# Performance work log

Measured on AMD Instinct MI355X. Metric: run time of the kernel, lower is better.

Reference implementation:

```python
import jax, jax.numpy as jnp
from jax import lax
import numpy as np

GRID = 16
N = GRID * GRID  # 256 nodes
D = 64           # embed_dim
CLIP = 3.0
EPS = 1e-8

def _grid_structs():
    mask = np.zeros((N, N), dtype=np.float32)
    first_nb = np.zeros(N, dtype=np.int64)
    for i in range(N):
        r, c = divmod(i, GRID)
        nbs = []
        if r > 0: nbs.append(i - GRID)
        if r < GRID - 1: nbs.append(i + GRID)
        if c > 0: nbs.append(i - 1)
        if c < GRID - 1: nbs.append(i + 1)
        for n in nbs:
            mask[i, n] = 1.0
        first_nb[i] = nbs[0]
    fn_onehot = np.zeros((N, N), dtype=bool)
    fn_onehot[np.arange(N), first_nb] = True
    return mask, fn_onehot

_ADJ_MASK_NP, _FN_ONEHOT_NP = _grid_structs()
_FN_ONEHOT = jnp.asarray(_FN_ONEHOT_NP)

def setup_inputs() -> dict:
    key = jax.random.key(0)
    ks = jax.random.split(key, 12)
    B, F, H, C = 4096, 512, D * N, 1000
    s = lambda fan: 1.0 / np.sqrt(fan)
    return {
        'x': jax.random.normal(ks[0], (B, F), jnp.float32),
        'W_in': jax.random.normal(ks[1], (H, F), jnp.float32) * s(F),
        'b_in': jnp.zeros((H,), jnp.float32),
        'adj_weights': jax.random.normal(ks[2], (N, N), jnp.float32) * 0.1,
        'adj_mask': jnp.asarray(_ADJ_MASK_NP),
        'V_slow': jax.random.normal(ks[3], (D, D), jnp.float32) * 0.1,
        'sem_mem': jax.random.normal(ks[4], (D, D), jnp.float32) * 0.01,
        'mix_w': jax.random.normal(ks[5], (1, D), jnp.float32) * s(D),
        'mix_b': jnp.zeros((1,), jnp.float32),
        'basis': jax.random.normal(ks[6], (4, D), jnp.float32) * 0.5,
        'q_w': jax.random.normal(ks[7], (D, D), jnp.float32) * s(D),
        'q_b': jnp.zeros((D,), jnp.float32),
        'k_w': jax.random.normal(ks[8], (D, D), jnp.float32) * s(D),
        'k_b': jnp.zeros((D,), jnp.float32),
        'W_out': jax.random.normal(ks[9], (C, H), jnp.float32) * s(H),
        'b_out': jnp.zeros((C,), jnp.float32),
    }

def reference(x, W_in, b_in, adj_weights, adj_mask, V_slow, sem_mem,
              mix_w, mix_b, basis, q_w, q_b, k_w, k_b, W_out, b_out):
    B = x.shape[0]
    # input embedding -> [B, N, D] node states
    nodes = (x @ W_in.T + b_in).reshape(B, N, D)

    # --- StableTopologyManager.get_adjacency (plasticity = 1.0) ---
    adj = jax.nn.sigmoid(adj_weights) * adj_mask          # [N, N]
    deg = jnp.clip(adj.sum(1, keepdims=True), 1e-6, None)
    adj = adj / deg
    # min-connections survival protocol (vectorized)
    need = (adj > 0.1).sum(1) < 1                         # [N]
    adj = jnp.where(need[:, None] & _FN_ONEHOT, jnp.maximum(adj, 0.5), adj)

    # grid message passing: aggregate neighbor states
    nodes = jnp.einsum('nm,bmd->bnd', adj, nodes)

    # --- StableContinuumMemoryCell (output path; EMA state update is no_grad
    # and does not affect this forward's output) ---
    v = jnp.clip(nodes @ V_slow.T, -CLIP, CLIP)
    y_pred = jnp.clip(nodes @ sem_mem.T, -CLIP, CLIP)
    v_pred = jnp.clip(y_pred @ V_slow.T, -CLIP, CLIP)
    mix = jax.nn.sigmoid(lax.stop_gradient(v) @ mix_w.T + mix_b)  # [B,N,1]
    cell_out = jnp.clip(mix * v + (1.0 - mix) * v_pred, -CLIP, CLIP)

    # --- StableSymbioticBasisRefinement ---
    Q = cell_out @ q_w.T + q_b                            # [B,N,D]
    K = basis @ k_w.T + k_b                               # [4,D]
    attn = (Q @ K.T) / (D ** 0.5 + EPS)                   # [B,N,4]
    w = jax.nn.softmax(attn, axis=-1)
    x_clean = jnp.clip(w @ basis, -3.0, 3.0)              # [B,N,D]

    # readout
    flat = x_clean.reshape(B, N * D)
    logits = flat @ W_out.T + b_out                       # [B, 1000]
    return logits
```

## Files before the change

kernel.cpp:

```cpp
#include <hip/hip_runtime.h>
#include <stdint.h>
#include <stddef.h>


typedef __attribute__((ext_vector_type(8))) __bf16 bf16x8;
typedef __attribute__((ext_vector_type(4))) float  floatx4;

#define N_NODES 256
#define F_IN    512
#define B_BATCH 4096
#define C_OUT   1000
#define NT      9
#define SCOLS   (N_NODES * NT)
#define KPACK   (N_NODES * 4)
#define OUT_N   4096000

__device__ __forceinline__ unsigned short f2us(float f) {
  unsigned int v; __builtin_memcpy(&v, &f, sizeof(v));
  unsigned int r = (v + 0x7FFFu + ((v >> 16) & 1u)) >> 16;
  return (unsigned short)r;
}
__device__ __forceinline__ float us2f(unsigned short u) {
  unsigned int v = ((unsigned int)u) << 16;
  float f; __builtin_memcpy(&f, &v, sizeof(f)); return f;
}
__device__ __forceinline__ void async_ld16(const void* g, void* l) {
  __builtin_amdgcn_global_load_lds(
      (const __attribute__((address_space(1))) unsigned int*)g,
      (__attribute__((address_space(3))) unsigned int*)l, 16, 0, 0);
}

__global__ __launch_bounds__(256)
void setup_kernel(const float* __restrict__ adj_w,
                  const float* __restrict__ basis,
                  const float* __restrict__ q_w,
                  const float* __restrict__ q_b,
                  const float* __restrict__ k_w,
                  const float* __restrict__ k_b,
                  const float* __restrict__ V_slow,
                  const float* __restrict__ sem_mem,
                  const float* __restrict__ mix_w,
                  const float* __restrict__ mix_b,
                  const float* __restrict__ b_in,
                  const float* __restrict__ b_out,
                  float* __restrict__ adjw, int* __restrict__ adjidx,
                  float* __restrict__ vecs,
                  float* __restrict__ qbK,
                  float* __restrict__ misc,
                  float* __restrict__ bias9,
                  float* __restrict__ biasc)
{
  __shared__ float K4[4 * 64];
  __shared__ float KQ[4 * 64];
  __shared__ float A1s[4 * 64];
  __shared__ float vecsS[9 * 64];
  __shared__ float adjwS[256 * 4];
  __shared__ int   adjidxS[256 * 4];
  const int tid = threadIdx.x;

  for (int i = tid; i < C_OUT; i += 256) biasc[i] = b_out[i];

  {
    const int n = tid, r = n >> 4, c = n & 15;
    int nb[4]; int cnt = 0;
    if (r > 0)  nb[cnt++] = n - 16;
    if (r < 15) nb[cnt++] = n + 16;
    if (c > 0)  nb[cnt++] = n - 1;
    if (c < 15) nb[cnt++] = n + 1;
    float wv[4] = {0.f, 0.f, 0.f, 0.f};
    float s = 0.f;
    for (int i = 0; i < cnt; ++i) {
      float sg = 1.f / (1.f + expf(-adj_w[(size_t)n * 256 + nb[i]]));
      wv[i] = sg; s += sg;
    }
    float deg = fmaxf(s, 1e-6f);
    int over = 0;
    for (int i = 0; i < cnt; ++i) { wv[i] /= deg; over += (wv[i] > 0.1f) ? 1 : 0; }
    if (over < 1) wv[0] = fmaxf(wv[0], 0.5f);
    for (int i = cnt; i < 4; ++i) nb[i] = n;
    for (int i = 0; i < 4; ++i) {
      adjw[n * 4 + i] = wv[i];  adjidx[n * 4 + i] = nb[i];
      adjwS[n * 4 + i] = wv[i]; adjidxS[n * 4 + i] = nb[i];
    }
  }
  {
    const int j = tid >> 6, d = tid & 63;
    float acc = k_b[d];
    for (int e = 0; e < 64; ++e) acc += basis[j * 64 + e] * k_w[d * 64 + e];
    K4[j * 64 + d] = acc;
  }
  __syncthreads();
  {
    const int j = tid >> 6, e = tid & 63;
    float acc = 0.f;
    for (int d = 0; d < 64; ++d) acc += K4[j * 64 + d] * q_w[d * 64 + e];
    KQ[j * 64 + e] = acc;
    if (tid < 4) {
      float q = 0.f;
      for (int d = 0; d < 64; ++d) q += q_b[d] * K4[tid * 64 + d];
      qbK[tid] = q;
    }
    if (tid == 0) misc[0] = mix_b[0];
  }
  __syncthreads();
  {
    const int j = tid >> 6, e = tid & 63;
    float acc = 0.f;
    for (int d = 0; d < 64; ++d) acc += KQ[j * 64 + d] * V_slow[d * 64 + e];
    A1s[j * 64 + e] = acc;
    vecsS[j * 64 + e] = acc;
    if (tid < 64) {
      float mm = 0.f;
      for (int d = 0; d < 64; ++d) mm += mix_w[d] * V_slow[d * 64 + tid];
      vecsS[8 * 64 + tid] = mm;
    }
  }
  __syncthreads();
  {
    const int j = tid >> 6, f = tid & 63;
    float acc = 0.f;
    for (int e = 0; e < 64; ++e) acc += A1s[j * 64 + e] * sem_mem[e * 64 + f];
    vecsS[(4 + j) * 64 + f] = acc;
  }
  __syncthreads();
  for (int i = tid; i < NT * 64; i += 256) vecs[i] = vecsS[i];
  {
    const int n = tid;
    float bt[9] = {0,0,0,0,0,0,0,0,0};
    for (int d = 0; d < 64; ++d) {
      float v = 0.f;
      for (int k = 0; k < 4; ++k)
        v += adjwS[n * 4 + k] * b_in[(size_t)adjidxS[n * 4 + k] * 64 + d];
      #pragma unroll
      for (int t = 0; t < 9; ++t) bt[t] += v * vecsS[t * 64 + d];
    }
    for (int t = 0; t < 9; ++t) bias9[n * 9 + t] = bt[t];
  }
}

__global__ __launch_bounds__(256)
void convert_x_kernel(const float* __restrict__ x, unsigned short* __restrict__ xb)
{
  const size_t i0 = ((size_t)blockIdx.x * 256 + threadIdx.x) * 8;
  const float4 a = *(const float4*)(x + i0);
  const float4 b = *(const float4*)(x + i0 + 4);
  ushort4 o0, o1;
  o0.x = f2us(a.x); o0.y = f2us(a.y); o0.z = f2us(a.z); o0.w = f2us(a.w);
  o1.x = f2us(b.x); o1.y = f2us(b.y); o1.z = f2us(b.z); o1.w = f2us(b.w);
  *(ushort4*)(xb + i0)     = o0;
  *(ushort4*)(xb + i0 + 4) = o1;
}

__global__ __launch_bounds__(512)
void build_T_kernel(const float* __restrict__ W_in,
                    const float* __restrict__ vecs,
                    float* __restrict__ T)
{
  __shared__ float vl[NT * 64];
  const int m = blockIdx.x, f = threadIdx.x;
  for (int i = threadIdx.x; i < NT * 64; i += 512) vl[i] = vecs[i];
  __syncthreads();
  float acc[NT] = {0,0,0,0,0,0,0,0,0};
  for (int d = 0; d < 64; ++d) {
    float wv = W_in[(size_t)(m * 64 + d) * F_IN + f];
    #pragma unroll
    for (int t = 0; t < NT; ++t) acc[t] += wv * vl[t * 64 + d];
  }
  for (int t = 0; t < NT; ++t) T[(size_t)(m * NT + t) * F_IN + f] = acc[t];
}

__global__ __launch_bounds__(512)
void build_U_kernel(const float* __restrict__ T,
                    const float* __restrict__ adjw,
                    const int* __restrict__ adjidx,
                    unsigned short* __restrict__ U)
{
  const int n = blockIdx.x, f = threadIdx.x;
  const float w0 = adjw[n * 4 + 0], w1 = adjw[n * 4 + 1];
  const float w2 = adjw[n * 4 + 2], w3 = adjw[n * 4 + 3];
  const int i0 = adjidx[n * 4 + 0], i1 = adjidx[n * 4 + 1];
  const int i2 = adjidx[n * 4 + 2], i3 = adjidx[n * 4 + 3];
  #pragma unroll
  for (int t = 0; t < NT; ++t) {
    float u = w0 * T[(size_t)(i0 * NT + t) * F_IN + f]
            + w1 * T[(size_t)(i1 * NT + t) * F_IN + f]
            + w2 * T[(size_t)(i2 * NT + t) * F_IN + f]
            + w3 * T[(size_t)(i3 * NT + t) * F_IN + f];
    U[(size_t)(n * NT + t) * F_IN + f] = f2us(u);
  }
}

__global__ __launch_bounds__(256)
void build_PT_kernel(const float* __restrict__ W_out,
                     const float* __restrict__ basis,
                     unsigned short* __restrict__ PT)
{
  const int c = blockIdx.x, tid = threadIdx.x;
  if (c >= C_OUT) {
    for (int i = tid; i < KPACK; i += 256) PT[(size_t)c * KPACK + i] = 0;
    return;
  }
  __shared__ __align__(16) float row[16384];
  __shared__ float bas[4 * 64];
  const float4* src = (const float4*)(W_out + (size_t)c * 16384);
  float4* dst = (float4*)row;
  for (int i = tid; i < 4096; i += 256) dst[i] = src[i];
  bas[tid] = basis[tid];
  __syncthreads();
  const int n = tid;
  float a0 = 0.f, a1 = 0.f, a2 = 0.f, a3 = 0.f;
  for (int dd = 0; dd < 64; ++dd) {
    int d = (dd + n) & 63;
    float wv = row[n * 64 + d];
    a0 += wv * bas[0 * 64 + d];
    a1 += wv * bas[1 * 64 + d];
    a2 += wv * bas[2 * 64 + d];
    a3 += wv * bas[3 * 64 + d];
  }
  unsigned short* p = PT + (size_t)c * KPACK + n * 4;
  p[0] = f2us(a0); p[1] = f2us(a1); p[2] = f2us(a2); p[3] = f2us(a3);
}

template <int K, bool FINAL>
__global__ __launch_bounds__(256)
void gemm_bt(const unsigned short* __restrict__ A,
             const unsigned short* __restrict__ B,
             unsigned short* __restrict__ Cb, float* __restrict__ Cf,
             int ncol, const float* __restrict__ biasf)
{
  __shared__ __align__(16) unsigned short As[2][128 * 64];
  __shared__ __align__(16) unsigned short Bs[2][64 * 64];
  const int tid  = threadIdx.x;
  const int lane = tid & 63;
  const int wave = tid >> 6;
  const int m0 = blockIdx.x * 128;
  const int n0 = blockIdx.y * 64;
  const int wm = (wave >> 1) * 64;
  const int wn = (wave & 1) * 32;

  floatx4 acc[4][2];
  #pragma unroll
  for (int i = 0; i < 4; ++i)
    #pragma unroll
    for (int j = 0; j < 2; ++j) acc[i][j] = (floatx4){0.f, 0.f, 0.f, 0.f};

  const int NK = K / 64;
  int cur = 0;

  auto stage = [&](int s, int kt) {
    const int k0 = kt * 64;
    #pragma unroll
    for (int it = 0; it < 4; ++it) {
      const int chunk = it * 256 + tid;
      async_ld16(A + (size_t)(m0 + (chunk >> 3)) * K + k0 + ((chunk & 7) << 3),
                 &As[s][(it * 256 + wave * 64) * 8]);
    }
    #pragma unroll
    for (int it = 0; it < 2; ++it) {
      const int chunk = it * 256 + tid;
      async_ld16(B + (size_t)(n0 + (chunk >> 3)) * K + k0 + ((chunk & 7) << 3),
                 &Bs[s][(it * 256 + wave * 64) * 8]);
    }
  };

  stage(0, 0);
  __syncthreads();

  for (int kt = 0; kt < NK; ++kt) {
    if (kt + 1 < NK) stage(cur ^ 1, kt + 1);
    const int lrow = lane & 15;
    #pragma unroll
    for (int kk = 0; kk < 2; ++kk) {
      const int lk = kk * 32 + (lane >> 4) * 8;
      bf16x8 af[4], bfr[2];
      #pragma unroll
      for (int i = 0; i < 4; ++i)
        af[i] = *(const bf16x8*)&As[cur][(wm + i * 16 + lrow) * 64 + lk];
      #pragma unroll
      for (int j = 0; j < 2; ++j)
        bfr[j] = *(const bf16x8*)&Bs[cur][(wn + j * 16 + lrow) * 64 + lk];
      #pragma unroll
      for (int i = 0; i < 4; ++i)
        #pragma unroll
        for (int j = 0; j < 2; ++j)
          acc[i][j] = __builtin_amdgcn_mfma_f32_16x16x32_bf16(af[i], bfr[j], acc[i][j], 0, 0, 0);
    }
    if (kt + 1 < NK) {
      __syncthreads();
      cur ^= 1;
    }
  }

  const int rq = (lane >> 4) * 4;
  const int cq = lane & 15;
  #pragma unroll
  for (int j = 0; j < 2; ++j) {
    const int col = n0 + wn + j * 16 + cq;
    if (FINAL && col >= ncol) continue;
    const float bv2 = FINAL ? biasf[col] : 0.f;
    #pragma unroll
    for (int i = 0; i < 4; ++i)
      #pragma unroll
      for (int r = 0; r < 4; ++r) {
        const int rowi = m0 + wm + i * 16 + rq + r;
        if (FINAL) Cf[(size_t)rowi * ncol + col] = acc[i][j][r] + bv2;
        else       Cb[(size_t)rowi * ncol + col] = f2us(acc[i][j][r]);
      }
  }
}

__global__ __launch_bounds__(256)
void softmax_kernel(const unsigned short* __restrict__ scores,
                    const float* __restrict__ bias9,
                    const float* __restrict__ qbK,
                    const float* __restrict__ misc,
                    unsigned short* __restrict__ w)
{
  const int b = blockIdx.x, n = threadIdx.x;
  const unsigned short* s = scores + (size_t)b * SCOLS + n * NT;
  const float* bs = bias9 + n * NT;
  const float mixb = misc[0];
  const float q0 = qbK[0], q1 = qbK[1], q2 = qbK[2], q3 = qbK[3];
  const float mix = 1.f / (1.f + expf(-(us2f(s[8]) + bs[8] + mixb)));
  const float om = 1.f - mix;
  const float inv_s = 1.f / (8.f + 1e-8f);
  float a0 = (mix * (us2f(s[0]) + bs[0]) + om * (us2f(s[4]) + bs[4]) + q0) * inv_s;
  float a1 = (mix * (us2f(s[1]) + bs[1]) + om * (us2f(s[5]) + bs[5]) + q1) * inv_s;
  float a2 = (mix * (us2f(s[2]) + bs[2]) + om * (us2f(s[6]) + bs[6]) + q2) * inv_s;
  float a3 = (mix * (us2f(s[3]) + bs[3]) + om * (us2f(s[7]) + bs[7]) + q3) * inv_s;
  const float mx = fmaxf(fmaxf(a0, a1), fmaxf(a2, a3));
  const float e0 = expf(a0 - mx), e1 = expf(a1 - mx);
  const float e2 = expf(a2 - mx), e3 = expf(a3 - mx);
  const float rs = 1.f / (e0 + e1 + e2 + e3);
  ushort4 pk;
  pk.x = f2us(e0 * rs); pk.y = f2us(e1 * rs);
  pk.z = f2us(e2 * rs); pk.w = f2us(e3 * rs);
  *(ushort4*)(w + (size_t)b * KPACK + n * 4) = pk;
}

__global__ __launch_bounds__(256)
void sentinel_kernel(float* __restrict__ out, float val) {
  const size_t i = (size_t)blockIdx.x * 256 + threadIdx.x;
  if (i < OUT_N) out[i] = val;
}

extern "C" void kernel_launch(void* const* d_in, const int* in_sizes, int n_in,
                              void* d_out, int out_size, void* d_ws, size_t ws_size,
                              hipStream_t stream)
{
  static const int EXP[16] = {2097152, 8388608, 16384, 65536, 65536, 4096, 4096,
                              64, 1, 256, 4096, 64, 4096, 64, 16384000, 1000};
  bool ok = (n_in == 16) && (out_size == OUT_N);
  if (ok) for (int i = 0; i < 16; ++i) ok = ok && (in_sizes[i] == EXP[i]);
  float* out32 = (float*)d_out;
  if (!ok) {
    sentinel_kernel<<<dim3(16000), dim3(256), 0, stream>>>(out32, 8192.f);
    return;
  }

  const float* x_f    = (const float*)d_in[0];
  const float* Win_f  = (const float*)d_in[1];
  const float* bin_f  = (const float*)d_in[2];
  const float* adjW_f = (const float*)d_in[3];
  const float* Vs_f   = (const float*)d_in[5];
  const float* sem_f  = (const float*)d_in[6];
  const float* mw_f   = (const float*)d_in[7];
  const float* mb_f   = (const float*)d_in[8];
  const float* bas_f  = (const float*)d_in[9];
  const float* qw_f   = (const float*)d_in[10];
  const float* qb_f   = (const float*)d_in[11];
  const float* kw_f   = (const float*)d_in[12];
  const float* kb_f   = (const float*)d_in[13];
  const float* Wout_f = (const float*)d_in[14];
  const float* bout_f = (const float*)d_in[15];

  int BCH = 1024;
  {
    auto need = [](size_t b) {
      size_t ts = 4718592 > 4608 * b ? 4718592 : 4608 * b;
      return (size_t)32768 + 2359296 + 2097152 + ts + 1024 * b + 2048 * b;
    };
    if (ws_size >= need(4096)) BCH = 4096;
    else if (ws_size >= need(2048)) BCH = 2048;
  }
  const int NCH = B_BATCH / BCH;
  if (ws_size < (size_t)12353536) {
    sentinel_kernel<<<dim3(16000), dim3(256), 0, stream>>>(
        out32, 16.f * (float)(ws_size >> 20));
    return;
  }

  uint8_t* ws = (uint8_t*)d_ws;
  float* adjw   = (float*)(ws + 0);
  int*   adjidx = (int*)  (ws + 4096);
  float* vecs   = (float*)(ws + 8192);
  float* qbK    = (float*)(ws + 10496);
  float* misc   = (float*)(ws + 10560);
  float* bias9  = (float*)(ws + 12288);
  float* biasc  = (float*)(ws + 21504);
  size_t off = 32768;
  unsigned short* U  = (unsigned short*)(ws + off); off += 2359296;
  unsigned short* PT = (unsigned short*)(ws + off); off += 2097152;
  float*          T  = (float*)(ws + off);
  unsigned short* sc = (unsigned short*)(ws + off);
  off += (4718592 > (size_t)4608 * BCH ? 4718592 : (size_t)4608 * BCH);
  unsigned short* xb = (unsigned short*)(ws + off); off += (size_t)1024 * BCH;
  unsigned short* wq = (unsigned short*)(ws + off);

  setup_kernel<<<dim3(1), dim3(256), 0, stream>>>(
      adjW_f, bas_f, qw_f, qb_f, kw_f, kb_f, Vs_f, sem_f, mw_f, mb_f,
      bin_f, bout_f, adjw, adjidx, vecs, qbK, misc, bias9, biasc);
  build_T_kernel<<<dim3(256), dim3(512), 0, stream>>>(Win_f, vecs, T);
  build_U_kernel<<<dim3(256), dim3(512), 0, stream>>>(T, adjw, adjidx, U);
  build_PT_kernel<<<dim3(1024), dim3(256), 0, stream>>>(Wout_f, bas_f, PT);

  for (int ch = 0; ch < NCH; ++ch) {
    const size_t row0 = (size_t)ch * BCH;
    convert_x_kernel<<<dim3(BCH / 4), dim3(256), 0, stream>>>(
        x_f + row0 * F_IN, xb);
    gemm_bt<F_IN, false><<<dim3(BCH / 128, SCOLS / 64), dim3(256), 0, stream>>>(
        xb, U, sc, nullptr, SCOLS, nullptr);
    softmax_kernel<<<dim3(BCH), dim3(256), 0, stream>>>(sc, bias9, qbK, misc, wq);
    gemm_bt<KPACK, true><<<dim3(BCH / 128, KPACK / 64), dim3(256), 0, stream>>>(
        wq, PT, nullptr, out32 + row0 * C_OUT, C_OUT, biasc);
  }
}
```

Before: 249.2 us.

## XOR-swizzle LDS tiles and use partial vmcnt waits for true double buffering

The GEMM's async global-to-LDS loads now use an XOR swizzle on the 16-byte chunk index, and the LDS fragment reads apply the same swizzle. This is meant to avoid bank conflicts in the ds_read pattern. The single __syncthreads after staging is replaced by an explicit s_waitcnt vmcnt(6) that waits only for the current tile while the next tile's loads stay in flight, followed by a raw s_barrier. This lets loads overlap compute, but it depends on the exact count of outstanding memory ops, so a compiler change in instruction count could break correctness.

```diff
diff --git a/kernel.cpp b/kernel.cpp
--- a/kernel.cpp
+++ b/kernel.cpp
@@ -245,40 +245,53 @@
     for (int j = 0; j < 2; ++j) acc[i][j] = (floatx4){0.f, 0.f, 0.f, 0.f};
 
   const int NK = K / 64;
-  int cur = 0;
 
   auto stage = [&](int s, int kt) {
     const int k0 = kt * 64;
     #pragma unroll
     for (int it = 0; it < 4; ++it) {
       const int chunk = it * 256 + tid;
-      async_ld16(A + (size_t)(m0 + (chunk >> 3)) * K + k0 + ((chunk & 7) << 3),
+      const int r = chunk >> 3, g = chunk & 7;
+      async_ld16(A + (size_t)(m0 + r) * K + k0 + ((g ^ (r & 7)) << 3),
                  &As[s][(it * 256 + wave * 64) * 8]);
     }
     #pragma unroll
     for (int it = 0; it < 2; ++it) {
       const int chunk = it * 256 + tid;
-      async_ld16(B + (size_t)(n0 + (chunk >> 3)) * K + k0 + ((chunk & 7) << 3),
+      const int r = chunk >> 3, g = chunk & 7;
+      async_ld16(B + (size_t)(n0 + r) * K + k0 + ((g ^ (r & 7)) << 3),
                  &Bs[s][(it * 256 + wave * 64) * 8]);
     }
   };
 
   stage(0, 0);
-  __syncthreads();
+  int cur = 0;
 
   for (int kt = 0; kt < NK; ++kt) {
-    if (kt + 1 < NK) stage(cur ^ 1, kt + 1);
+    if (kt + 1 < NK) {
+      stage(cur ^ 1, kt + 1);
+      asm volatile("s_waitcnt vmcnt(6)" ::: "memory");
+    } else {
+      asm volatile("s_waitcnt vmcnt(0)" ::: "memory");
+    }
+    __builtin_amdgcn_s_barrier();
+
     const int lrow = lane & 15;
+    const int ghi  = lane >> 4;
     #pragma unroll
     for (int kk = 0; kk < 2; ++kk) {
-      const int lk = kk * 32 + (lane >> 4) * 8;
+      const int gbase = kk * 4 + ghi;
       bf16x8 af[4], bfr[2];
       #pragma unroll
-      for (int i = 0; i < 4; ++i)
-        af[i] = *(const bf16x8*)&As[cur][(wm + i * 16 + lrow) * 64 + lk];
+      for (int i = 0; i < 4; ++i) {
+        const int row = wm + i * 16 + lrow;
+        af[i] = *(const bf16x8*)&As[cur][row * 64 + ((gbase ^ (row & 7)) << 3)];
+      }
       #pragma unroll
-      for (int j = 0; j < 2; ++j)
-        bfr[j] = *(const bf16x8*)&Bs[cur][(wn + j * 16 + lrow) * 64 + lk];
+      for (int j = 0; j < 2; ++j) {
+        const int row = wn + j * 16 + lrow;
+        bfr[j] = *(const bf16x8*)&Bs[cur][row * 64 + ((gbase ^ (row & 7)) << 3)];
+      }
       #pragma unroll
       for (int i = 0; i < 4; ++i)
         #pragma unroll
@@ -286,7 +299,7 @@
           acc[i][j] = __builtin_amdgcn_mfma_f32_16x16x32_bf16(af[i], bfr[j], acc[i][j], 0, 0, 0);
     }
     if (kt + 1 < NK) {
-      __syncthreads();
+      __builtin_amdgcn_s_barrier();
       cur ^= 1;
     }
   }
```

New measurement: 243.7 us. -2.2%, faster.
